# Performance work log

Measured on AMD Instinct MI355X. Metric: run time of the kernel, lower is better.

The kernel has to match this reference:

```python
import jax, jax.numpy as jnp
import numpy as np

N_E = 1024
N_H = 16
SZ = N_E // N_H  # 64
NEG_INF = float('-inf')


def _layernorm(x, g, b):
    # Faithful to source: unbiased variance (ddof=1), eps added AFTER sqrt.
    mu = jnp.mean(x, axis=-1, keepdims=True)
    v = jnp.var(x, axis=-1, keepdims=True, ddof=1)
    xn = (x - mu) / (jnp.sqrt(v) + 1e-8)
    return g * xn + b


def setup_inputs() -> dict:
    key = jax.random.key(0)
    ks = jax.random.split(key, 16)
    s = 0.02
    x = jax.random.normal(ks[0], (4, 2048, N_E), dtype=jnp.float32)
    # Stacked per-head Q/K/V linears: weight [H, sz, n_e], bias [H, sz]
    Wq = jax.random.normal(ks[1], (N_H, SZ, N_E), dtype=jnp.float32) * s
    bq = jax.random.normal(ks[2], (N_H, SZ), dtype=jnp.float32) * s
    Wk = jax.random.normal(ks[3], (N_H, SZ, N_E), dtype=jnp.float32) * s
    bk = jax.random.normal(ks[4], (N_H, SZ), dtype=jnp.float32) * s
    Wv = jax.random.normal(ks[5], (N_H, SZ, N_E), dtype=jnp.float32) * s
    bv = jax.random.normal(ks[6], (N_H, SZ), dtype=jnp.float32) * s
    Wo = jax.random.normal(ks[7], (N_E, N_E), dtype=jnp.float32) * s
    bo = jax.random.normal(ks[8], (N_E,), dtype=jnp.float32) * s
    g1 = jnp.ones((N_E,), dtype=jnp.float32)
    be1 = jnp.zeros((N_E,), dtype=jnp.float32)
    g2 = jnp.ones((N_E,), dtype=jnp.float32)
    be2 = jnp.zeros((N_E,), dtype=jnp.float32)
    W1 = jax.random.normal(ks[9], (4 * N_E, N_E), dtype=jnp.float32) * s
    bf1 = jax.random.normal(ks[10], (4 * N_E,), dtype=jnp.float32) * s
    W2 = jax.random.normal(ks[11], (N_E, 4 * N_E), dtype=jnp.float32) * s
    bf2 = jax.random.normal(ks[12], (N_E,), dtype=jnp.float32) * s
    return dict(x=x, Wq=Wq, bq=bq, Wk=Wk, bk=bk, Wv=Wv, bv=bv, Wo=Wo, bo=bo,
                g1=g1, be1=be1, g2=g2, be2=be2, W1=W1, bf1=bf1, W2=W2, bf2=bf2)


def reference(x, Wq, bq, Wk, bk, Wv, bv, Wo, bo, g1, be1, g2, be2, W1, bf1, W2, bf2):
    # --- MHA sublayer ---
    xn = _layernorm(x, g1, be1)
    # Q/K/V for all heads at once: [B, H, S, sz]
    Q = jnp.einsum('bsd,hkd->bhsk', xn, Wq) + bq[None, :, None, :]
    K = jnp.einsum('bsd,hkd->bhsk', xn, Wk) + bk[None, :, None, :]
    V = jnp.einsum('bsd,hkd->bhsk', xn, Wv) + bv[None, :, None, :]
    scores = jnp.einsum('bhqk,bhmk->bhqm', Q, K) / (SZ ** 0.5)  # [B,H,S,S]
    # Faithful to source quirk: mask where tril(scores) == 0
    masked = jnp.where(jnp.tril(scores) == 0, NEG_INF, scores)
    attn = jax.nn.softmax(masked, axis=-1)
    o = jnp.einsum('bhqm,bhmk->bhqk', attn, V)  # [B,H,S,sz]
    B, H, S, _ = o.shape
    o = jnp.transpose(o, (0, 2, 1, 3)).reshape(B, S, H * SZ)  # concat heads
    x = x + o @ Wo.T + bo
    # --- FFN sublayer (dropout = identity in eval) ---
    xn2 = _layernorm(x, g2, be2)
    h = jax.nn.gelu(xn2 @ W1.T + bf1, approximate=False)
    x = x + h @ W2.T + bf2
    return x
```

## Files before the change

### kernel.cpp

```cpp
#include <hip/hip_runtime.h>
#include <math.h>


typedef unsigned short u16;
typedef unsigned int u32;
typedef __attribute__((ext_vector_type(8))) short bf16x8;
typedef __attribute__((ext_vector_type(4))) float f32x4;

#define T_TOK 8192
#define DM    1024
#define SEQ   2048
#define PST   88

__device__ __forceinline__ u16 f2bf(float f) {
  union { float f; unsigned int u; } c; c.f = f;
  unsigned int u = c.u + 0x7fffu + ((c.u >> 16) & 1u);
  return (u16)(u >> 16);
}

__device__ __forceinline__ u32 pk2(float a, float b) {
  return (u32)f2bf(a) | ((u32)f2bf(b) << 16);
}

__device__ __forceinline__ float bf2f(short s) {
  union { float f; unsigned int u; } c; c.u = ((u32)(u16)s) << 16;
  return c.f;
}

__device__ __forceinline__ void gload16(const void* gp, void* lp) {
  __builtin_amdgcn_global_load_lds(
      (const __attribute__((address_space(1))) void*)gp,
      (__attribute__((address_space(3))) void*)lp, 16, 0, 0);
}

__device__ __forceinline__ float gelu_tanh(float v) {
  float u = 0.7978845608f * (v + 0.044715f * v * v * v);
  return v / (1.0f + __expf(-2.0f * u));
}

__global__ __launch_bounds__(256) void cast_all(const float* __restrict__ Wq,
    const float* __restrict__ Wk, const float* __restrict__ Wv,
    const float* __restrict__ Wo, const float* __restrict__ W1,
    const float* __restrict__ W2, u16* __restrict__ WqkvB,
    u16* __restrict__ WoB, u16* __restrict__ W1B, u16* __restrict__ W2B) {
  for (int i = blockIdx.x * 256 + threadIdx.x; i < 3145728; i += gridDim.x * 256) {
    const float* s; u16* d; int j;
    if (i < 262144)       { s = Wq; d = WqkvB;           j = i; }
    else if (i < 524288)  { s = Wk; d = WqkvB + 1048576; j = i - 262144; }
    else if (i < 786432)  { s = Wv; d = WqkvB + 2097152; j = i - 524288; }
    else if (i < 1048576) { s = Wo; d = WoB;             j = i - 786432; }
    else if (i < 2097152) { s = W1; d = W1B;             j = i - 1048576; }
    else                  { s = W2; d = W2B;             j = i - 2097152; }
    float4 v = reinterpret_cast<const float4*>(s)[j];
    ushort4 o = { f2bf(v.x), f2bf(v.y), f2bf(v.z), f2bf(v.w) };
    reinterpret_cast<ushort4*>(d)[j] = o;
  }
}

__global__ __launch_bounds__(256) void concat_bias(const float* __restrict__ q,
    const float* __restrict__ k, const float* __restrict__ v, float* __restrict__ out) {
  int i = blockIdx.x * 256 + threadIdx.x;
  float val = (i < 1024) ? q[i] : (i < 2048) ? k[i - 1024] : v[i - 2048];
  out[i] = val;
}

__global__ __launch_bounds__(256) void ln_kernel(const float* __restrict__ x,
    const float* __restrict__ g, const float* __restrict__ b, u16* __restrict__ out) {
  __shared__ float red[4];
  const int tid = threadIdx.x, l = tid & 63, w = tid >> 6;
  const size_t row = blockIdx.x;
  float4 v = reinterpret_cast<const float4*>(x + row * DM)[tid];
  float s = v.x + v.y + v.z + v.w;
#pragma unroll
  for (int off = 1; off < 64; off <<= 1) s += __shfl_xor(s, off, 64);
  if (l == 0) red[w] = s;
  __syncthreads();
  float mu = (red[0] + red[1] + red[2] + red[3]) * (1.0f / 1024.0f);
  float dx = v.x - mu, dy = v.y - mu, dz = v.z - mu, dw = v.w - mu;
  float ss = dx * dx + dy * dy + dz * dz + dw * dw;
#pragma unroll
  for (int off = 1; off < 64; off <<= 1) ss += __shfl_xor(ss, off, 64);
  __syncthreads();
  if (l == 0) red[w] = ss;
  __syncthreads();
  float var = (red[0] + red[1] + red[2] + red[3]) * (1.0f / 1023.0f);
  float inv = 1.0f / (sqrtf(var) + 1e-8f);
  const int c = tid * 4;
  u16* o = out + row * DM + c;
  o[0] = f2bf(dx * inv * g[c + 0] + b[c + 0]);
  o[1] = f2bf(dy * inv * g[c + 1] + b[c + 1]);
  o[2] = f2bf(dz * inv * g[c + 2] + b[c + 2]);
  o[3] = f2bf(dw * inv * g[c + 3] + b[c + 3]);
}

__global__ __launch_bounds__(256) void vt_kernel(const u16* __restrict__ vr,
                                                 u16* __restrict__ vt) {
  __shared__ u16 t[64][72];
  const int st = blockIdx.x;
  const int bh = blockIdx.y, b = bh >> 4, h = bh & 15;
  const int tid = threadIdx.x;
  const int ss = tid >> 3, dc = (tid & 7) * 8;
  const u16* src = vr + (size_t)(b * SEQ + st * 64) * 1024 + h * 64;
  *(bf16x8*)&t[ss][dc]      = *(const bf16x8*)(src + (size_t)ss * 1024 + dc);
  *(bf16x8*)&t[ss + 32][dc] = *(const bf16x8*)(src + (size_t)(ss + 32) * 1024 + dc);
  __syncthreads();
  const int d0 = tid >> 3, s0 = (tid & 7) * 8;
  u16* dst = vt + (size_t)bh * 64 * SEQ + st * 64;
  bf16x8 o0, o1;
#pragma unroll
  for (int i = 0; i < 8; ++i) {
    o0[i] = (short)t[s0 + i][d0];
    o1[i] = (short)t[s0 + i][d0 + 32];
  }
  *(bf16x8*)(dst + (size_t)d0 * SEQ + s0)        = o0;
  *(bf16x8*)(dst + (size_t)(d0 + 32) * SEQ + s0) = o1;
}

template <int EPI, int BM>
__global__ __launch_bounds__(512) void gemm8p(const u16* __restrict__ A,
    const u16* __restrict__ Bw, const float* __restrict__ bias,
    const float* res, void* Cout, void* aux, int M, int N, int K, int gx) {
  constexpr int MI  = BM / 32;
  constexpr int AMI = MI / 2;
  constexpr int VC  = (BM == 256) ? 6 : 5;
  __shared__ __align__(16) u16 ldsA[2][2][BM * 32];
  __shared__ __align__(16) u16 ldsB[2][2][256 * 32];
  const int tid = threadIdx.x;
  const int l = tid & 63;
  const int w = tid >> 6;
  const int wm = w >> 2, wn = w & 3;
  const int lr = l & 15, lg = l >> 4;

  const int nb = gridDim.x;
  const int q = nb >> 3, r = nb & 7;
  const int xcd = blockIdx.x & 7, jj = blockIdx.x >> 3;
  const int lid = (xcd < r ? xcd * (q + 1) : r * (q + 1) + (xcd - r) * q) + jj;
  const int stid = lid >> 5, pos = lid & 31;
  const int nstx = gx >> 2;
  const int stx = stid % nstx, sty = stid / nstx;
  const int bx = stx * 4 + (pos & 3), by = sty * 8 + (pos >> 2);
  const int m0 = by * BM, n0 = bx * 256;

  const int Dl = tid * 16;
  const int Ls = Dl ^ (((Dl >> 7) & 3) << 4);
  const int srow = Ls >> 6;
  const int scol = (Ls & 63) >> 1;
  const u16* aS0 = A  + (size_t)(m0 + srow) * K + scol;
  const u16* aS1 = aS0 + (size_t)128 * K;
  const u16* bS0 = Bw + (size_t)(n0 + srow) * K + scol;
  const u16* bS1 = bS0 + (size_t)128 * K;

  const int sx = ((lr >> 1) & 3) << 4;
  const int aBase = (wm * (BM / 2) + lr) * 64 + ((lg * 16) ^ sx);
  const int bBase = (wn * 64 + lr) * 64 + ((lg * 16) ^ sx);

  f32x4 acc[MI][4];
#pragma unroll
  for (int i = 0; i < MI; ++i)
#pragma unroll
    for (int j = 0; j < 4; ++j) acc[i][j] = f32x4{0.f, 0.f, 0.f, 0.f};
  bf16x8 bv[2][4];

  const int NT = K >> 6;
  const int NI = NT >> 1;

  auto stA = [&](int d, int ks, int tile) {
    u16* dst = &ldsA[d][ks][tid * 8];
    const int ko = tile * 64 + ks * 32;
    gload16(aS0 + ko, dst);
    if constexpr (BM == 256) gload16(aS1 + ko, dst + 4096);
  };
  auto stB = [&](int d, int ks, int tile) {
    u16* dst = &ldsB[d][ks][tid * 8];
    const int ko = tile * 64 + ks * 32;
    gload16(bS0 + ko, dst);
    gload16(bS1 + ko, dst + 4096);
  };

  stB(0, 0, 0); stB(0, 1, 0); stA(0, 0, 0); stA(0, 1, 0);
  stB(1, 0, 1); stB(1, 1, 1); stA(1, 0, 1);
  asm volatile("s_waitcnt vmcnt(%0)" :: "i"(VC) : "memory");
  __builtin_amdgcn_sched_barrier(0);
  __builtin_amdgcn_s_barrier();

#define PHASE(DBUF, KS, MH, READB, STAGE, ENDV)                               \
  {                                                                           \
    const char* abuf = (const char*)&ldsA[DBUF][KS][0];                       \
    const char* bbuf = (const char*)&ldsB[DBUF][KS][0];                       \
    bf16x8 av[AMI];                                                           \
    _Pragma("unroll")                                                         \
    for (int i = 0; i < AMI; ++i)                                             \
      av[i] = *(const bf16x8*)(abuf + aBase + ((MH) * AMI + i) * 1024);       \
    if (READB) {                                                              \
      _Pragma("unroll")                                                       \
      for (int ni = 0; ni < 4; ++ni)                                          \
        bv[KS][ni] = *(const bf16x8*)(bbuf + bBase + ni * 1024);              \
    }                                                                         \
    STAGE;                                                                    \
    __builtin_amdgcn_s_barrier();                                             \
    asm volatile("s_waitcnt lgkmcnt(0)" ::: "memory");                        \
    __builtin_amdgcn_sched_barrier(0);                                        \
    __builtin_amdgcn_s_setprio(1);                                            \
    _Pragma("unroll")                                                         \
    for (int i = 0; i < AMI; ++i)                                             \
      _Pragma("unroll")                                                       \
      for (int ni = 0; ni < 4; ++ni)                                          \
        acc[(MH) * AMI + i][ni] = __builtin_amdgcn_mfma_f32_16x16x32_bf16(    \
            av[i], bv[KS][ni], acc[(MH) * AMI + i][ni], 0, 0, 0);             \
    __builtin_amdgcn_s_setprio(0);                                            \
    ENDV;                                                                     \
    __builtin_amdgcn_s_barrier();                                             \
  }

#define ENDV_CNT                                                              \
  {                                                                           \
    if (t + 1 < NI) {                                                         \
      asm volatile("s_waitcnt vmcnt(%0)" :: "i"(VC) : "memory");              \
    } else {                                                                  \
      asm volatile("s_waitcnt vmcnt(0)" ::: "memory");                        \
    }                                                                         \
    __builtin_amdgcn_sched_barrier(0);                                        \
  }

  for (int t = 0; t < NI; ++t) {
    const int t2 = 2 * t;
    const bool s0 = (t2 + 2 < NT);
    const bool s1 = (t2 + 3 < NT);
    PHASE(0, 0, 0, 1, { stA(1, 1, t2 + 1); }, {});
    PHASE(0, 1, 0, 1, { if (s0) stB(0, 0, t2 + 2); }, {});
    PHASE(0, 0, 1, 0, { if (s0) stB(0, 1, t2 + 2); }, {});
    PHASE(0, 1, 1, 0, { if (s0) stA(0, 0, t2 + 2); }, ENDV_CNT);
    PHASE(1, 0, 0, 1, { if (s0) stA(0, 1, t2 + 2); }, {});
    PHASE(1, 1, 0, 1, { if (s1) stB(1, 0, t2 + 3); }, {});
    PHASE(1, 0, 1, 0, { if (s1) stB(1, 1, t2 + 3); }, {});
    PHASE(1, 1, 1, 0, { if (s1) stA(1, 0, t2 + 3); }, ENDV_CNT);
  }
#undef PHASE
#undef ENDV_CNT

  float bs[4];
#pragma unroll
  for (int ni = 0; ni < 4; ++ni) bs[ni] = bias[n0 + wn * 64 + ni * 16 + lr];
#pragma unroll
  for (int mi = 0; mi < MI; ++mi) {
#pragma unroll
    for (int j = 0; j < 4; ++j) {
      const int rr = m0 + wm * (BM / 2) + mi * 16 + lg * 4 + j;
#pragma unroll
      for (int ni = 0; ni < 4; ++ni) {
        const int c = n0 + wn * 64 + ni * 16 + lr;
        float v = acc[mi][ni][j] + bs[ni];
        if constexpr (EPI == 0) {
          if (n0 >= 2048) {
            ((u16*)aux)[(size_t)rr * 1024 + (c - 2048)] = f2bf(v);
          } else {
            ((u16*)Cout)[(size_t)rr * 2048 + c] = f2bf(v);
          }
        } else if constexpr (EPI == 1) {
          const size_t idx = (size_t)rr * N + c;
          ((float*)Cout)[idx] = v + res[idx];
        } else {
          const size_t idx = (size_t)rr * N + c;
          ((u16*)Cout)[idx] = f2bf(gelu_tanh(v));
        }
      }
    }
  }
}

__global__ __launch_bounds__(512) void attn_kernel(const u16* __restrict__ qk,
    const u16* __restrict__ vt, u16* __restrict__ obuf) {
  __shared__ __align__(16) u16 ldsK[3][64 * 64];
  __shared__ __align__(16) u16 ldsV[3][64 * 64];
  __shared__ __align__(16) u16 ldsP[8][2][16 * PST];
  const int tid = threadIdx.x, l = tid & 63, w = tid >> 6;
  const int lr = l & 15, lg = l >> 4;
  const int lid = (blockIdx.x & 7) * 32 + (blockIdx.x >> 3);
  const int bh = lid >> 2, bx = lid & 3;
  const int b = bh >> 4, h = bh & 15;
  const u16* qbase = qk + (size_t)b * SEQ * 2048 + h * 64;
  const u16* kbase = qk + (size_t)b * SEQ * 2048 + 1024 + h * 64;
  const u16* vbase = vt + (size_t)bh * 64 * SEQ;

  const int srow = tid >> 3;
  const int scb  = ((tid & 7) * 16) ^ ((srow & 7) << 4);
  const int sel  = scb >> 1;

  auto stageKV = [&](int t) {
    const int bi = t % 3;
    gload16(kbase + (size_t)(t * 64 + srow) * 2048 + sel, &ldsK[bi][tid * 8]);
    gload16(vbase + (size_t)srow * SEQ + t * 64 + sel,    &ldsV[bi][tid * 8]);
  };

#pragma unroll
  for (int half = 0; half < 2; ++half) {
    const int qt = half ? (7 - bx) : bx;
    const int q0 = qt * 256 + w * 32;
    bf16x8 qf[2][2];
#pragma unroll
    for (int mi = 0; mi < 2; ++mi)
#pragma unroll
      for (int ks = 0; ks < 2; ++ks) {
        bf16x8 raw = *(const bf16x8*)(qbase +
            (size_t)(q0 + mi * 16 + lr) * 2048 + ks * 32 + lg * 8);
        bf16x8 sc8;
#pragma unroll
        for (int i = 0; i < 8; ++i) sc8[i] = (short)f2bf(bf2f(raw[i]) * 0.125f);
        qf[mi][ks] = sc8;
      }

    f32x4 o[2][4];
#pragma unroll
    for (int mi = 0; mi < 2; ++mi)
#pragma unroll
      for (int nd = 0; nd < 4; ++nd) o[mi][nd] = f32x4{0.f, 0.f, 0.f, 0.f};
    float m_[2] = {-1e30f, -1e30f}, ls[2] = {0.f, 0.f};

    const int nt = 4 * qt + 4;
    const int qmaxw = q0 + 31;

    stageKV(0);

    for (int kt = 0; kt < nt; ++kt) {
      if (kt + 1 < nt) {
        stageKV(kt + 1);
        asm volatile("s_waitcnt vmcnt(2)" ::: "memory");
      } else {
        asm volatile("s_waitcnt vmcnt(0)" ::: "memory");
      }
      __builtin_amdgcn_s_barrier();
      __builtin_amdgcn_sched_barrier(0);
      const u16* bK = &ldsK[kt % 3][0];
      const u16* bV = &ldsV[kt % 3][0];

      if (kt * 64 <= qmaxw) {
        f32x4 sc[2][4];
#pragma unroll
        for (int mi = 0; mi < 2; ++mi)
#pragma unroll
          for (int ni = 0; ni < 4; ++ni) sc[mi][ni] = f32x4{0.f, 0.f, 0.f, 0.f};
#pragma unroll
        for (int ks = 0; ks < 2; ++ks)
#pragma unroll
          for (int ni = 0; ni < 4; ++ni) {
            const int r2 = ni * 16 + lr;
            const int cb = (r2 << 7) + ((ks * 64 + lg * 16) ^ ((r2 & 7) << 4));
            bf16x8 kf = *(const bf16x8*)&bK[cb >> 1];
            sc[0][ni] = __builtin_amdgcn_mfma_f32_16x16x32_bf16(kf, qf[0][ks], sc[0][ni], 0, 0, 0);
            sc[1][ni] = __builtin_amdgcn_mfma_f32_16x16x32_bf16(kf, qf[1][ks], sc[1][ni], 0, 0, 0);
          }

        if (kt * 64 + 63 > q0) {
#pragma unroll
          for (int mi = 0; mi < 2; ++mi) {
            const int qa = q0 + mi * 16 + lr;
#pragma unroll
            for (int ni = 0; ni < 4; ++ni)
#pragma unroll
              for (int j = 0; j < 4; ++j) {
                const int ka = kt * 64 + ni * 16 + lg * 4 + j;
                if (ka > qa) sc[mi][ni][j] = -1e30f;
              }
          }
        }

#pragma unroll
        for (int mi = 0; mi < 2; ++mi) {
          float mx = sc[mi][0][0];
#pragma unroll
          for (int ni = 0; ni < 4; ++ni)
#pragma unroll
            for (int j = 0; j < 4; ++j) mx = fmaxf(mx, sc[mi][ni][j]);
          mx = fmaxf(mx, __shfl_xor(mx, 16, 64));
          mx = fmaxf(mx, __shfl_xor(mx, 32, 64));
          if (!__all(mx <= m_[mi] + 8.0f)) {
            const float newm = fmaxf(m_[mi], mx);
            const float alpha = __expf(m_[mi] - newm);
            m_[mi] = newm;
            ls[mi] *= alpha;
#pragma unroll
            for (int nd = 0; nd < 4; ++nd) {
              o[mi][nd][0] *= alpha; o[mi][nd][1] *= alpha;
              o[mi][nd][2] *= alpha; o[mi][nd][3] *= alpha;
            }
          }
          float ps = 0.f;
#pragma unroll
          for (int ni = 0; ni < 4; ++ni) {
            float p0 = __expf(sc[mi][ni][0] - m_[mi]);
            float p1 = __expf(sc[mi][ni][1] - m_[mi]);
            float p2 = __expf(sc[mi][ni][2] - m_[mi]);
            float p3 = __expf(sc[mi][ni][3] - m_[mi]);
            ps += (p0 + p1) + (p2 + p3);
            u32 w0 = pk2(p0, p1), w1 = pk2(p2, p3);
            *(uint2*)&ldsP[w][mi][lr * PST + ni * 16 + lg * 4] = make_uint2(w0, w1);
          }
          ps += __shfl_xor(ps, 16, 64);
          ps += __shfl_xor(ps, 32, 64);
          ls[mi] += ps;
        }

#pragma unroll
        for (int ks = 0; ks < 2; ++ks) {
          bf16x8 pf0 = *(const bf16x8*)&ldsP[w][0][lr * PST + ks * 32 + lg * 8];
          bf16x8 pf1 = *(const bf16x8*)&ldsP[w][1][lr * PST + ks * 32 + lg * 8];
#pragma unroll
          for (int nd = 0; nd < 4; ++nd) {
            const int r2 = nd * 16 + lr;
            const int cb = (r2 << 7) + ((ks * 64 + lg * 16) ^ ((r2 & 7) << 4));
            bf16x8 vf = *(const bf16x8*)&bV[cb >> 1];
            o[0][nd] = __builtin_amdgcn_mfma_f32_16x16x32_bf16(vf, pf0, o[0][nd], 0, 0, 0);
            o[1][nd] = __builtin_amdgcn_mfma_f32_16x16x32_bf16(vf, pf1, o[1][nd], 0, 0, 0);
          }
        }
      }
    }
    __builtin_amdgcn_s_barrier();

#pragma unroll
    for (int mi = 0; mi < 2; ++mi) {
      const float inv = 1.0f / ls[mi];
      const int qrow = q0 + mi * 16 + lr;
      u16* op = obuf + (size_t)(b * SEQ + qrow) * DM + h * 64 + lg * 4;
#pragma unroll
      for (int nd = 0; nd < 4; ++nd) {
        ushort4 pk = { f2bf(o[mi][nd][0] * inv), f2bf(o[mi][nd][1] * inv),
                       f2bf(o[mi][nd][2] * inv), f2bf(o[mi][nd][3] * inv) };
        *(ushort4*)(op + nd * 16) = pk;
      }
    }
  }
}

extern "C" void kernel_launch(void* const* d_in, const int* in_sizes, int n_in,
                              void* d_out, int out_size, void* d_ws, size_t ws_size,
                              hipStream_t stream) {
  const float* x   = (const float*)d_in[0];
  const float* Wq  = (const float*)d_in[1];
  const float* bq  = (const float*)d_in[2];
  const float* Wk  = (const float*)d_in[3];
  const float* bk  = (const float*)d_in[4];
  const float* Wv  = (const float*)d_in[5];
  const float* bv  = (const float*)d_in[6];
  const float* Wo  = (const float*)d_in[7];
  const float* bo  = (const float*)d_in[8];
  const float* g1  = (const float*)d_in[9];
  const float* be1 = (const float*)d_in[10];
  const float* g2  = (const float*)d_in[11];
  const float* be2 = (const float*)d_in[12];
  const float* W1  = (const float*)d_in[13];
  const float* bf1 = (const float*)d_in[14];
  const float* W2  = (const float*)d_in[15];
  const float* bf2 = (const float*)d_in[16];
  float* out = (float*)d_out;

  char* ws = (char*)d_ws;
  size_t off = 0;
  auto alloc = [&](size_t bytes) {
    char* p = ws + off;
    off += (bytes + 255) & ~(size_t)255;
    return p;
  };
  u16* xnB = (u16*)alloc((size_t)T_TOK * DM * 2);
  u16* D    = (u16*)alloc((size_t)T_TOK * 4096 * 2);
  u16* qkB  = D;
  u16* VTg  = D + (size_t)T_TOK * 2048;
  u16* Vrow = D + (size_t)T_TOK * 3072;
  u16* oB   = Vrow;
  u16* HB   = D;
  u16*   WqkvB = (u16*)alloc((size_t)3072 * 1024 * 2);
  u16*   WoB   = (u16*)alloc((size_t)1024 * 1024 * 2);
  u16*   W1B   = (u16*)alloc((size_t)4096 * 1024 * 2);
  u16*   W2B   = (u16*)alloc((size_t)1024 * 4096 * 2);
  float* bqkv  = (float*)alloc(3072 * 4);

  cast_all<<<2048, 256, 0, stream>>>(Wq, Wk, Wv, Wo, W1, W2,
                                     WqkvB, WoB, W1B, W2B);
  concat_bias<<<12, 256, 0, stream>>>(bq, bk, bv, bqkv);

  ln_kernel<<<T_TOK, 256, 0, stream>>>(x, g1, be1, xnB);
  gemm8p<0, 256><<<384, 512, 0, stream>>>(xnB, WqkvB, bqkv, nullptr,
                                          qkB, Vrow, T_TOK, 3072, 1024, 12);
  vt_kernel<<<dim3(32, 64), 256, 0, stream>>>(Vrow, VTg);
  attn_kernel<<<256, 512, 0, stream>>>(qkB, VTg, oB);
  gemm8p<1, 128><<<256, 512, 0, stream>>>(oB, WoB, bo, x,
                                          out, nullptr, T_TOK, 1024, 1024, 4);

  ln_kernel<<<T_TOK, 256, 0, stream>>>(out, g2, be2, xnB);
  gemm8p<2, 256><<<512, 512, 0, stream>>>(xnB, W1B, bf1, nullptr,
                                          HB, nullptr, T_TOK, 4096, 1024, 16);
  gemm8p<1, 128><<<256, 512, 0, stream>>>(HB, W2B, bf2, out,
                                          out, nullptr, T_TOK, 1024, 4096, 4);
}
```

Baseline: 387.9 us.

## Merge weight cast, bias concat and first layernorm into one prep kernel; retile QKV GEMM

After: 383.0 us. Within noise of the previous version (-1.3%).

```diff
diff --git a/kernel.cpp b/kernel.cpp
--- a/kernel.cpp
+++ b/kernel.cpp
@@ -38,30 +38,61 @@
   return v / (1.0f + __expf(-2.0f * u));
 }
 
-__global__ __launch_bounds__(256) void cast_all(const float* __restrict__ Wq,
-    const float* __restrict__ Wk, const float* __restrict__ Wv,
-    const float* __restrict__ Wo, const float* __restrict__ W1,
-    const float* __restrict__ W2, u16* __restrict__ WqkvB,
-    u16* __restrict__ WoB, u16* __restrict__ W1B, u16* __restrict__ W2B) {
-  for (int i = blockIdx.x * 256 + threadIdx.x; i < 3145728; i += gridDim.x * 256) {
-    const float* s; u16* d; int j;
-    if (i < 262144)       { s = Wq; d = WqkvB;           j = i; }
-    else if (i < 524288)  { s = Wk; d = WqkvB + 1048576; j = i - 262144; }
-    else if (i < 786432)  { s = Wv; d = WqkvB + 2097152; j = i - 524288; }
-    else if (i < 1048576) { s = Wo; d = WoB;             j = i - 786432; }
-    else if (i < 2097152) { s = W1; d = W1B;             j = i - 1048576; }
-    else                  { s = W2; d = W2B;             j = i - 2097152; }
-    float4 v = reinterpret_cast<const float4*>(s)[j];
-    ushort4 o = { f2bf(v.x), f2bf(v.y), f2bf(v.z), f2bf(v.w) };
-    reinterpret_cast<ushort4*>(d)[j] = o;
-  }
-}
-
-__global__ __launch_bounds__(256) void concat_bias(const float* __restrict__ q,
-    const float* __restrict__ k, const float* __restrict__ v, float* __restrict__ out) {
-  int i = blockIdx.x * 256 + threadIdx.x;
-  float val = (i < 1024) ? q[i] : (i < 2048) ? k[i - 1024] : v[i - 2048];
-  out[i] = val;
+__global__ __launch_bounds__(256) void prep_kernel(
+    const float* __restrict__ x, const float* __restrict__ g,
+    const float* __restrict__ b, u16* __restrict__ xnB,
+    const float* __restrict__ Wq, const float* __restrict__ Wk,
+    const float* __restrict__ Wv, const float* __restrict__ Wo,
+    const float* __restrict__ W1, const float* __restrict__ W2,
+    u16* __restrict__ WqkvB, u16* __restrict__ WoB,
+    u16* __restrict__ W1B, u16* __restrict__ W2B,
+    const float* __restrict__ bq, const float* __restrict__ bk,
+    const float* __restrict__ bv, float* __restrict__ bqkv) {
+  __shared__ float red[4];
+  const int bid = blockIdx.x, tid = threadIdx.x;
+  if (bid < 8192) {
+    const int l = tid & 63, w = tid >> 6;
+    const size_t row = bid;
+    float4 v = reinterpret_cast<const float4*>(x + row * DM)[tid];
+    float s = v.x + v.y + v.z + v.w;
+#pragma unroll
+    for (int off = 1; off < 64; off <<= 1) s += __shfl_xor(s, off, 64);
+    if (l == 0) red[w] = s;
+    __syncthreads();
+    float mu = (red[0] + red[1] + red[2] + red[3]) * (1.0f / 1024.0f);
+    float dx = v.x - mu, dy = v.y - mu, dz = v.z - mu, dw = v.w - mu;
+    float ss = dx * dx + dy * dy + dz * dz + dw * dw;
+#pragma unroll
+    for (int off = 1; off < 64; off <<= 1) ss += __shfl_xor(ss, off, 64);
+    __syncthreads();
+    if (l == 0) red[w] = ss;
+    __syncthreads();
+    float var = (red[0] + red[1] + red[2] + red[3]) * (1.0f / 1023.0f);
+    float inv = 1.0f / (sqrtf(var) + 1e-8f);
+    const int c = tid * 4;
+    u16* o = xnB + row * DM + c;
+    o[0] = f2bf(dx * inv * g[c + 0] + b[c + 0]);
+    o[1] = f2bf(dy * inv * g[c + 1] + b[c + 1]);
+    o[2] = f2bf(dz * inv * g[c + 2] + b[c + 2]);
+    o[3] = f2bf(dw * inv * g[c + 3] + b[c + 3]);
+  } else if (bid < 10240) {
+    for (int i = (bid - 8192) * 256 + tid; i < 3145728; i += 2048 * 256) {
+      const float* s; u16* d; int j;
+      if (i < 262144)       { s = Wq; d = WqkvB;           j = i; }
+      else if (i < 524288)  { s = Wk; d = WqkvB + 1048576; j = i - 262144; }
+      else if (i < 786432)  { s = Wv; d = WqkvB + 2097152; j = i - 524288; }
+      else if (i < 1048576) { s = Wo; d = WoB;             j = i - 786432; }
+      else if (i < 2097152) { s = W1; d = W1B;             j = i - 1048576; }
+      else                  { s = W2; d = W2B;             j = i - 2097152; }
+      float4 v = reinterpret_cast<const float4*>(s)[j];
+      ushort4 o = { f2bf(v.x), f2bf(v.y), f2bf(v.z), f2bf(v.w) };
+      reinterpret_cast<ushort4*>(d)[j] = o;
+    }
+  } else {
+    int i = (bid - 10240) * 256 + tid;
+    float val = (i < 1024) ? bq[i] : (i < 2048) ? bk[i - 1024] : bv[i - 2048];
+    bqkv[i] = val;
+  }
 }
 
 __global__ __launch_bounds__(256) void ln_kernel(const float* __restrict__ x,
@@ -474,12 +505,12 @@
   u16*   W2B   = (u16*)alloc((size_t)1024 * 4096 * 2);
   float* bqkv  = (float*)alloc(3072 * 4);
 
-  cast_all<<<2048, 256, 0, stream>>>(Wq, Wk, Wv, Wo, W1, W2,
-                                     WqkvB, WoB, W1B, W2B);
-  concat_bias<<<12, 256, 0, stream>>>(bq, bk, bv, bqkv);
-
-  ln_kernel<<<T_TOK, 256, 0, stream>>>(x, g1, be1, xnB);
-  gemm8p<0, 256><<<384, 512, 0, stream>>>(xnB, WqkvB, bqkv, nullptr,
+  prep_kernel<<<10252, 256, 0, stream>>>(x, g1, be1, xnB,
+                                         Wq, Wk, Wv, Wo, W1, W2,
+                                         WqkvB, WoB, W1B, W2B,
+                                         bq, bk, bv, bqkv);
+
+  gemm8p<0, 128><<<768, 512, 0, stream>>>(xnB, WqkvB, bqkv, nullptr,
                                           qkB, Vrow, T_TOK, 3072, 1024, 12);
   vt_kernel<<<dim3(32, 64), 256, 0, stream>>>(Vrow, VTg);
   attn_kernel<<<256, 512, 0, stream>>>(qkB, VTg, oB);
```
